# Optimization experiments

Hardware: AMD Instinct MI355X
Metric: run time of the kernel (lower is better)

## Reference

```python
import jax, jax.numpy as jnp
import numpy as np
import math

V, P, D, L, H = 50257, 1024, 768, 12, 12
HD = D // H
DFF = 4 * D
B, S = 2, 1024
EPS = 1e-5


def setup_inputs() -> dict:
    key = jax.random.key(0)
    ks = jax.random.split(key, 8)
    sc = 0.02
    return {
        "input_ids": jax.random.randint(ks[0], (B, S), 0, V),
        "wte": jax.random.normal(ks[1], (V, D), jnp.float32) * sc,
        "wpe": jax.random.normal(ks[2], (P, D), jnp.float32) * sc,
        "ln1_g": jnp.ones((L, D), jnp.float32),
        "ln1_b": jnp.zeros((L, D), jnp.float32),
        "qkv_w": jax.random.normal(ks[3], (L, 3 * D, D), jnp.float32) * sc,
        "qkv_b": jnp.zeros((L, 3 * D), jnp.float32),
        "proj_w": jax.random.normal(ks[4], (L, D, D), jnp.float32) * sc,
        "proj_b": jnp.zeros((L, D), jnp.float32),
        "ln2_g": jnp.ones((L, D), jnp.float32),
        "ln2_b": jnp.zeros((L, D), jnp.float32),
        "fc_w": jax.random.normal(ks[5], (L, DFF, D), jnp.float32) * sc,
        "fc_b": jnp.zeros((L, DFF), jnp.float32),
        "cproj_w": jax.random.normal(ks[6], (L, D, DFF), jnp.float32) * sc,
        "cproj_b": jnp.zeros((L, D), jnp.float32),
        "lnf_g": jnp.ones((D,), jnp.float32),
        "lnf_b": jnp.zeros((D,), jnp.float32),
    }


def layer_norm(x, g, b):
    mu = jnp.mean(x, axis=-1, keepdims=True)
    var = jnp.mean(jnp.square(x - mu), axis=-1, keepdims=True)
    return (x - mu) * jax.lax.rsqrt(var + EPS) * g + b


def _forward(input_ids, wte, wpe, ln1_g, ln1_b, qkv_w, qkv_b, proj_w, proj_b,
             ln2_g, ln2_b, fc_w, fc_b, cproj_w, cproj_b, lnf_g, lnf_b):
    s = input_ids.shape[1]
    h = wte[input_ids] + wpe[jnp.arange(s)][None, :, :]  # [B,S,D]
    causal = jnp.tril(jnp.ones((s, s), bool))  # [S,S]
    neg_inf = jnp.finfo(h.dtype).min

    def step(x, p):
        l1g, l1b, qw, qb, pw, pb, l2g, l2b, fw, fb, cw, cb = p
        hn = layer_norm(x, l1g, l1b)
        qkv = hn @ qw.T + qb  # [B,S,3D]
        q, k, v = jnp.split(qkv, 3, axis=-1)
        q = q.reshape(B, s, H, HD).transpose(0, 2, 1, 3)  # [B,H,S,hd]
        k = k.reshape(B, s, H, HD).transpose(0, 2, 1, 3)
        v = v.reshape(B, s, H, HD).transpose(0, 2, 1, 3)
        scores = jnp.einsum("bhqd,bhkd->bhqk", q, k) / math.sqrt(HD)
        scores = jnp.where(causal[None, None], scores, neg_inf)
        attn = jax.nn.softmax(scores, axis=-1)
        o = jnp.einsum("bhqk,bhkd->bhqd", attn, v)
        o = o.transpose(0, 2, 1, 3).reshape(B, s, D)
        x = x + (o @ pw.T + pb)
        hn2 = layer_norm(x, l2g, l2b)
        m = jax.nn.gelu(hn2 @ fw.T + fb, approximate=False)
        x = x + (m @ cw.T + cb)
        return x, None

    params = (ln1_g, ln1_b, qkv_w, qkv_b, proj_w, proj_b,
              ln2_g, ln2_b, fc_w, fc_b, cproj_w, cproj_b)
    h, _ = jax.lax.scan(step, h, params)
    h = layer_norm(h, lnf_g, lnf_b)
    logits = h @ wte.T  # tied lm_head, [B,S,V]
    return logits


def reference(input_ids, wte, wpe, ln1_g, ln1_b, qkv_w, qkv_b, proj_w, proj_b,
              ln2_g, ln2_b, fc_w, fc_b, cproj_w, cproj_b, lnf_g, lnf_b):
    return _forward(input_ids, wte, wpe, ln1_g, ln1_b, qkv_w, qkv_b, proj_w,
                    proj_b, ln2_g, ln2_b, fc_w, fc_b, cproj_w, cproj_b,
                    lnf_g, lnf_b)
```

## Files before the change

### kernel.cpp

```cpp
#include <hip/hip_runtime.h>

#define BB 2
#define SS 1024
#define DM 768
#define NH 12
#define HDIM 64
#define NL 12
#define DFFN 3072
#define VOC 50257
#define ROWS (BB * SS)
#define MT (ROWS / 128)

typedef __attribute__((ext_vector_type(4))) float f32x4;
typedef __attribute__((ext_vector_type(8))) short short8;
typedef __attribute__((ext_vector_type(4))) short short4v;
typedef unsigned short ushort;

__device__ __forceinline__ ushort f2bf(float f) {
  union { float f; unsigned int u; } x; x.f = f;
  unsigned int u = x.u;
  unsigned int r = (u + 0x7FFFu + ((u >> 16) & 1u)) >> 16;
  return (ushort)r;
}

__global__ __launch_bounds__(256) void embed_k(const int* __restrict__ ids,
    const float* __restrict__ wte, const float* __restrict__ wpe,
    float* __restrict__ h) {
  const int row = blockIdx.x;
  const int s = row & (SS - 1);
  const int tid = threadIdx.x;
  const int id = ids[row];
  const size_t wbase = (size_t)id * DM;
  const size_t pbase = (size_t)s * DM;
  const size_t obase = (size_t)row * DM;
  h[obase + tid]       = wte[wbase + tid]       + wpe[pbase + tid];
  h[obase + tid + 256] = wte[wbase + tid + 256] + wpe[pbase + tid + 256];
  h[obase + tid + 512] = wte[wbase + tid + 512] + wpe[pbase + tid + 512];
}

__global__ __launch_bounds__(256) void f2b_k(const float* __restrict__ in,
                                             ushort* __restrict__ out, int n4) {
  for (int i = blockIdx.x * 256 + threadIdx.x; i < n4; i += gridDim.x * 256) {
    f32x4 v = ((const f32x4*)in)[i];
    short4v s;
    s[0] = f2bf(v[0]); s[1] = f2bf(v[1]); s[2] = f2bf(v[2]); s[3] = f2bf(v[3]);
    ((short4v*)out)[i] = s;
  }
}

template <int OB>
__global__ __launch_bounds__(256) void layernorm_t(const float* __restrict__ x,
    const float* __restrict__ g, const float* __restrict__ b, void* __restrict__ y) {
  const int tid = threadIdx.x;
  const size_t base = (size_t)blockIdx.x * DM;
  float v0 = x[base + tid], v1 = x[base + tid + 256], v2 = x[base + tid + 512];
  __shared__ float red[256];
  red[tid] = v0 + v1 + v2;
  __syncthreads();
  for (int off = 128; off > 0; off >>= 1) {
    if (tid < off) red[tid] += red[tid + off];
    __syncthreads();
  }
  float mu = red[0] * (1.0f / DM);
  __syncthreads();
  float d0 = v0 - mu, d1 = v1 - mu, d2 = v2 - mu;
  red[tid] = d0 * d0 + d1 * d1 + d2 * d2;
  __syncthreads();
  for (int off = 128; off > 0; off >>= 1) {
    if (tid < off) red[tid] += red[tid + off];
    __syncthreads();
  }
  float rstd = rsqrtf(red[0] * (1.0f / DM) + 1e-5f);
  float o0 = d0 * rstd * g[tid]       + b[tid];
  float o1 = d1 * rstd * g[tid + 256] + b[tid + 256];
  float o2 = d2 * rstd * g[tid + 512] + b[tid + 512];
  if (OB) {
    ushort* yo = (ushort*)y;
    yo[base + tid] = f2bf(o0); yo[base + tid + 256] = f2bf(o1);
    yo[base + tid + 512] = f2bf(o2);
  } else {
    float* yo = (float*)y;
    yo[base + tid] = o0; yo[base + tid + 256] = o1; yo[base + tid + 512] = o2;
  }
}

template <int ROUNDS>
__device__ __forceinline__ void stage_sw(const ushort* __restrict__ g, int ldg,
                                         ushort* lds, int wave, int lane,
                                         int rowmax) {
#pragma unroll
  for (int r = 0; r < ROUNDS; r++) {
    const int chunk = (r * 4 + wave) * 64 + lane;
    const int nrow = chunk >> 3;
    const int cs = (chunk & 7) ^ (nrow & 7);
    const int row = nrow > rowmax ? rowmax : nrow;
    const ushort* ga = g + (size_t)row * ldg + cs * 8;
    ushort* la = lds + (r * 4 + wave) * 512;
    __builtin_amdgcn_global_load_lds(
        (const __attribute__((address_space(1))) unsigned int*)ga,
        (__attribute__((address_space(3))) unsigned int*)la, 16, 0, 0);
  }
}

__global__ __launch_bounds__(256) void gemm_lg(const ushort* __restrict__ A,
    const ushort* __restrict__ Bw, float* __restrict__ Cout, int N, int K) {
  __shared__ __align__(16) ushort smem[4 * 8192];
  ushort* AsL0 = smem;
  ushort* AsL1 = smem + 8192;
  ushort* BsL0 = smem + 16384;
  ushort* BsL1 = smem + 24576;

  const int tid = threadIdx.x;
  const int lane = tid & 63;
  const int wave = tid >> 6;
  const int la = lane & 15;
  const int hi = lane >> 4;
  const int swz = (la & 7) << 3;

  const int nwg = gridDim.x;
  int bid = blockIdx.x;
  {
    const int q = nwg >> 3, r = nwg & 7;
    const int xcd = bid & 7, idx = bid >> 3;
    bid = (xcd < r ? xcd * (q + 1) : r * (q + 1) + (xcd - r) * q) + idx;
  }
  const int m0 = (bid % MT) * 128;
  const int n0 = (bid / MT) * 128;

  const int wr = (wave >> 1) * 64;
  const int wc = (wave & 1) * 64;
  const int brmax = min(N - n0 - 1, 127);

  f32x4 acc[4][4];
#pragma unroll
  for (int i = 0; i < 4; i++)
#pragma unroll
    for (int j = 0; j < 4; j++) acc[i][j] = (f32x4){0.f, 0.f, 0.f, 0.f};

  const ushort* Ag = A + (size_t)m0 * K;
  const ushort* Bg = Bw + (size_t)n0 * K;

  const int nt = K >> 6;
  const int s0 = (bid % MT) % nt;

  stage_sw<4>(Ag + s0 * 64, K, AsL0, wave, lane, 127);
  stage_sw<4>(Bg + s0 * 64, K, BsL0, wave, lane, brmax);

  int cur = 0;
  for (int t = 0; t < nt; t++) {
    if (t + 1 < nt) {
      int sn = t + 1 + s0; if (sn >= nt) sn -= nt;
      stage_sw<4>(Ag + sn * 64, K, cur ? AsL0 : AsL1, wave, lane, 127);
      stage_sw<4>(Bg + sn * 64, K, cur ? BsL0 : BsL1, wave, lane, brmax);
      asm volatile("s_waitcnt vmcnt(8)" ::: "memory");
    } else {
      asm volatile("s_waitcnt vmcnt(0)" ::: "memory");
    }
    __builtin_amdgcn_s_barrier();
    __builtin_amdgcn_sched_barrier(0);

    const ushort* Ab = (cur ? AsL1 : AsL0) + (wr + la) * 64;
    const ushort* Bb = (cur ? BsL1 : BsL0) + (wc + la) * 64;
    __builtin_amdgcn_s_setprio(1);
#pragma unroll
    for (int ks = 0; ks < 2; ks++) {
      const int co = (ks * 32 + hi * 8) ^ swz;
      short8 a[4], b[4];
#pragma unroll
      for (int mi = 0; mi < 4; mi++)
        a[mi] = *(const short8*)(Ab + mi * 1024 + co);
#pragma unroll
      for (int ni = 0; ni < 4; ni++)
        b[ni] = *(const short8*)(Bb + ni * 1024 + co);
#pragma unroll
      for (int mi = 0; mi < 4; mi++)
#pragma unroll
        for (int ni = 0; ni < 4; ni++)
          acc[mi][ni] = __builtin_amdgcn_mfma_f32_16x16x32_bf16(
              a[mi], b[ni], acc[mi][ni], 0, 0, 0);
    }
    __builtin_amdgcn_s_setprio(0);
    __builtin_amdgcn_sched_barrier(0);
    __builtin_amdgcn_s_barrier();
    __builtin_amdgcn_sched_barrier(0);
    cur ^= 1;
  }

  float* L = (float*)smem;
  const int myhalf = wave & 1;
#pragma unroll
  for (int h = 0; h < 2; h++) {
    if (myhalf == h) {
#pragma unroll
      for (int mi = 0; mi < 4; mi++)
#pragma unroll
        for (int ni = 0; ni < 4; ni++)
#pragma unroll
          for (int j = 0; j < 4; j++) {
            const int row = wr + mi * 16 + 4 * hi + j;
            const int col = ni * 16 + la;
            L[row * 68 + col] = acc[mi][ni][j];
          }
    }
    __syncthreads();
#pragma unroll
    for (int it = 0; it < 32; it++) {
      const int flat = it * 256 + tid;
      const int row = flat >> 6, col = flat & 63;
      const int gc = n0 + h * 64 + col;
      if (gc < N)
        Cout[(size_t)(m0 + row) * N + gc] = L[row * 68 + col];
    }
    __syncthreads();
  }
}

template <int EPI, int OUTBF, int MR>
__global__ __launch_bounds__(256) void gemm_p3(const ushort* __restrict__ A,
    const ushort* __restrict__ Bw, const float* __restrict__ bias,
    const float* __restrict__ res, void* __restrict__ Cout, int N, int K) {
  constexpr int MROWS = MR * 32;
  constexpr int MTILES = ROWS / MROWS;
  constexpr int ASZ = MROWS * 64;
  constexpr int BSZ = 64 * 64;
  __shared__ __align__(16) ushort smem[3 * ASZ + 3 * BSZ];
  ushort* As = smem;
  ushort* Bs = smem + 3 * ASZ;

  const int tid = threadIdx.x;
  const int lane = tid & 63;
  const int wave = tid >> 6;
  const int la = lane & 15;
  const int hi = lane >> 4;
  const int swz = (la & 7) << 3;

  const int nwg = gridDim.x;
  int bid = blockIdx.x;
  {
    const int q = nwg >> 3, r = nwg & 7;
    const int xcd = bid & 7, idx = bid >> 3;
    bid = (xcd < r ? xcd * (q + 1) : r * (q + 1) + (xcd - r) * q) + idx;
  }
  const int m0 = (bid % MTILES) * MROWS;
  const int n0 = (bid / MTILES) * 64;

  const int wr = (wave >> 1) * (MROWS / 2);
  const int wc = (wave & 1) * 32;

  f32x4 acc[MR][2];
#pragma unroll
  for (int i = 0; i < MR; i++)
#pragma unroll
    for (int j = 0; j < 2; j++) acc[i][j] = (f32x4){0.f, 0.f, 0.f, 0.f};

  const ushort* Ag = A + (size_t)m0 * K;
  const ushort* Bg = Bw + (size_t)n0 * K;
  const int nt = K >> 6;
  const int s0 = (bid % MTILES) % nt;

  {
    int s1 = s0 + 1; if (s1 >= nt) s1 -= nt;
    stage_sw<MR>(Ag + s0 * 64, K, As, wave, lane, MROWS - 1);
    stage_sw<2>(Bg + s0 * 64, K, Bs, wave, lane, 63);
    stage_sw<MR>(Ag + s1 * 64, K, As + ASZ, wave, lane, MROWS - 1);
    stage_sw<2>(Bg + s1 * 64, K, Bs + BSZ, wave, lane, 63);
  }

  for (int t = 0; t < nt; t++) {
    if (t + 1 < nt) {
      asm volatile("s_waitcnt vmcnt(%0)" :: "i"(MR + 2) : "memory");
    } else {
      asm volatile("s_waitcnt vmcnt(0)" ::: "memory");
    }
    __builtin_amdgcn_s_barrier();
    __builtin_amdgcn_sched_barrier(0);

    const ushort* Ab = As + (t % 3) * ASZ + (wr + la) * 64;
    const ushort* Bb = Bs + (t % 3) * BSZ + (wc + la) * 64;
    __builtin_amdgcn_s_setprio(1);
#pragma unroll
    for (int ks = 0; ks < 2; ks++) {
      const int co = (ks * 32 + hi * 8) ^ swz;
      short8 a[MR], b[2];
#pragma unroll
      for (int mi = 0; mi < MR; mi++)
        a[mi] = *(const short8*)(Ab + mi * 1024 + co);
#pragma unroll
      for (int ni = 0; ni < 2; ni++)
        b[ni] = *(const short8*)(Bb + ni * 1024 + co);
#pragma unroll
      for (int mi = 0; mi < MR; mi++)
#pragma unroll
        for (int ni = 0; ni < 2; ni++)
          acc[mi][ni] = __builtin_amdgcn_mfma_f32_16x16x32_bf16(
              a[mi], b[ni], acc[mi][ni], 0, 0, 0);
    }
    __builtin_amdgcn_s_setprio(0);
    __builtin_amdgcn_sched_barrier(0);
    __builtin_amdgcn_s_barrier();
    __builtin_amdgcn_sched_barrier(0);
    if (t + 2 < nt) {
      int sn = t + 2 + s0; if (sn >= nt) sn -= nt;
      stage_sw<MR>(Ag + sn * 64, K, As + ((t + 2) % 3) * ASZ, wave, lane, MROWS - 1);
      stage_sw<2>(Bg + sn * 64, K, Bs + ((t + 2) % 3) * BSZ, wave, lane, 63);
    }
  }

  if (OUTBF) {
    ushort* L = smem;
#pragma unroll
    for (int mi = 0; mi < MR; mi++)
#pragma unroll
      for (int ni = 0; ni < 2; ni++)
#pragma unroll
        for (int j = 0; j < 4; j++) {
          const int row = wr + mi * 16 + 4 * hi + j;
          const int col = wc + ni * 16 + la;
          float x = acc[mi][ni][j];
          if (EPI >= 1) x += bias[n0 + col];
          if (EPI == 3) x = 0.5f * x * (1.0f + erff(x * 0.70710678118f));
          L[row * 72 + col] = f2bf(x);
        }
    __syncthreads();
    ushort* Co = (ushort*)Cout;
    constexpr int ITERS = MROWS * 64 / 8 / 256;
#pragma unroll
    for (int it = 0; it < ITERS; it++) {
      const int idx8 = it * 256 + tid;
      const int row = idx8 >> 3, c8 = idx8 & 7;
      short8 v = *(const short8*)&L[row * 72 + c8 * 8];
      *(short8*)&Co[(size_t)(m0 + row) * N + n0 + c8 * 8] = v;
    }
  } else {
    float* L = (float*)smem;
#pragma unroll
    for (int mi = 0; mi < MR; mi++)
#pragma unroll
      for (int ni = 0; ni < 2; ni++)
#pragma unroll
        for (int j = 0; j < 4; j++) {
          const int row = wr + mi * 16 + 4 * hi + j;
          const int col = wc + ni * 16 + la;
          float x = acc[mi][ni][j];
          if (EPI >= 1) x += bias[n0 + col];
          if (EPI == 3) x = 0.5f * x * (1.0f + erff(x * 0.70710678118f));
          L[row * 68 + col] = x;
        }
    __syncthreads();
    f32x4* Co = (f32x4*)Cout;
    const f32x4* R4 = (const f32x4*)res;
    constexpr int ITERS = MROWS * 64 / 4 / 256;
#pragma unroll
    for (int it = 0; it < ITERS; it++) {
      const int idx4 = it * 256 + tid;
      const int row = idx4 >> 4, c4 = idx4 & 15;
      f32x4 v = *(const f32x4*)&L[row * 68 + c4 * 4];
      const size_t o4 = ((size_t)(m0 + row) * N + n0) / 4 + c4;
      if (EPI == 2) v += R4[o4];
      Co[o4] = v;
    }
  }
}

__global__ __launch_bounds__(256) void attn_bf(const ushort* __restrict__ qkv,
                                               ushort* __restrict__ o) {
  const int tid = threadIdx.x;
  const int lane = tid & 63;
  const int wave = tid >> 6;
  const int hi = lane >> 4;
  const int la = lane & 15;
  const int q0 = blockIdx.x * 64;
  const int bh = blockIdx.y;
  const int bb = bh / NH;
  const int hh = bh % NH;
  const size_t rstride = 3 * DM;
  const ushort* base = qkv + (size_t)bb * SS * rstride;
  const ushort* kbase = base + DM + hh * HDIM;
  const ushort* vbase = base + 2 * DM + hh * HDIM;

  __shared__ ushort Ks[64][72];
  __shared__ ushort Vt[64][72];
  __shared__ ushort Pb[4][16][72];

  const int kr = tid >> 2;
  const int kc = (tid & 3) * 16;
  const int vp0 = (tid >> 3) * 2;
  const int vc = (tid & 7) * 8;

  short8 qf[2];
  {
    const int qrow = q0 + wave * 16 + la;
    const ushort* qp = base + (size_t)qrow * rstride + hh * HDIM + 8 * hi;
    qf[0] = *(const short8*)qp;
    qf[1] = *(const short8*)(qp + 32);
  }

  short8 kA, kB, vA, vB;
  {
    const ushort* kp = kbase + (size_t)kr * rstride + kc;
    kA = *(const short8*)kp;
    kB = *(const short8*)(kp + 8);
    const ushort* vp = vbase + (size_t)vp0 * rstride + vc;
    vA = *(const short8*)vp;
    vB = *(const short8*)(vp + rstride);
  }

  f32x4 accO[4] = {};
  float m_[4], l_[4];
#pragma unroll
  for (int j = 0; j < 4; j++) { m_[j] = -1e30f; l_[j] = 0.f; }

  const int nt = q0 / 64 + 1;
  for (int kt = 0; kt < nt; kt++) {
    __syncthreads();
    *(short8*)&Ks[kr][kc]     = kA;
    *(short8*)&Ks[kr][kc + 8] = kB;
#pragma unroll
    for (int i = 0; i < 8; i++) {
      unsigned int pk = (unsigned int)(unsigned short)vA[i] |
                        ((unsigned int)(unsigned short)vB[i] << 16);
      *(unsigned int*)&Vt[vc + i][vp0] = pk;
    }
    __syncthreads();
    if (kt + 1 < nt) {
      const ushort* kp = kbase + (size_t)((kt + 1) * 64 + kr) * rstride + kc;
      kA = *(const short8*)kp;
      kB = *(const short8*)(kp + 8);
      const ushort* vp = vbase + (size_t)((kt + 1) * 64 + vp0) * rstride + vc;
      vA = *(const short8*)vp;
      vB = *(const short8*)(vp + rstride);
    }

    f32x4 s[4] = {};
#pragma unroll
    for (int f = 0; f < 4; f++) {
#pragma unroll
      for (int kk = 0; kk < 2; kk++) {
        short8 kf = *(const short8*)&Ks[f * 16 + la][kk * 32 + 8 * hi];
        s[f] = __builtin_amdgcn_mfma_f32_16x16x32_bf16(qf[kk], kf, s[f], 0, 0, 0);
      }
#pragma unroll
      for (int j = 0; j < 4; j++) s[f][j] *= 0.125f;
    }

    if (kt == nt - 1) {
      const int qr = wave * 16 + 4 * hi;
#pragma unroll
      for (int f = 0; f < 4; f++) {
        const int kcol = f * 16 + la;
#pragma unroll
        for (int j = 0; j < 4; j++)
          if (kcol > qr + j) s[f][j] = -1e30f;
      }
    }

#pragma unroll
    for (int j = 0; j < 4; j++) {
      float rm = fmaxf(fmaxf(s[0][j], s[1][j]), fmaxf(s[2][j], s[3][j]));
      rm = fmaxf(rm, __shfl_xor(rm, 1));
      rm = fmaxf(rm, __shfl_xor(rm, 2));
      rm = fmaxf(rm, __shfl_xor(rm, 4));
      rm = fmaxf(rm, __shfl_xor(rm, 8));
      const float mnew = fmaxf(m_[j], rm);
      const float alpha = expf(m_[j] - mnew);
      float rs = 0.f;
#pragma unroll
      for (int f = 0; f < 4; f++) {
        const float p = expf(s[f][j] - mnew);
        s[f][j] = p;
        rs += p;
      }
      rs += __shfl_xor(rs, 1);
      rs += __shfl_xor(rs, 2);
      rs += __shfl_xor(rs, 4);
      rs += __shfl_xor(rs, 8);
      l_[j] = l_[j] * alpha + rs;
      m_[j] = mnew;
#pragma unroll
      for (int f = 0; f < 4; f++) accO[f][j] *= alpha;
    }

#pragma unroll
    for (int f = 0; f < 4; f++)
#pragma unroll
      for (int j = 0; j < 4; j++)
        Pb[wave][4 * hi + j][f * 16 + la] = f2bf(s[f][j]);

    short8 pf0 = *(const short8*)&Pb[wave][la][8 * hi];
    short8 pf1 = *(const short8*)&Pb[wave][la][32 + 8 * hi];
#pragma unroll
    for (int f = 0; f < 4; f++) {
      short8 vf0 = *(const short8*)&Vt[f * 16 + la][8 * hi];
      short8 vf1 = *(const short8*)&Vt[f * 16 + la][32 + 8 * hi];
      accO[f] = __builtin_amdgcn_mfma_f32_16x16x32_bf16(pf0, vf0, accO[f], 0, 0, 0);
      accO[f] = __builtin_amdgcn_mfma_f32_16x16x32_bf16(pf1, vf1, accO[f], 0, 0, 0);
    }
  }

  ushort* op = o + (size_t)(bb * SS + q0 + wave * 16) * DM + hh * HDIM;
#pragma unroll
  for (int j = 0; j < 4; j++) {
    const float inv = 1.0f / l_[j];
    const int qr = 4 * hi + j;
#pragma unroll
    for (int f = 0; f < 4; f++)
      op[(size_t)qr * DM + f * 16 + la] = f2bf(accO[f][j] * inv);
  }
}

template <int EPI>
__global__ __launch_bounds__(256) void gemm_nt(const float* __restrict__ A,
    const float* __restrict__ Bw, const float* __restrict__ bias,
    const float* __restrict__ res, float* __restrict__ C, int N, int K) {
  __shared__ ushort As[64][40];
  __shared__ ushort Bs[64][40];
  const int tid = threadIdx.x;
  const int m0 = blockIdx.y * 64;
  const int n0 = blockIdx.x * 64;
  const int lane = tid & 63;
  const int wave = tid >> 6;
  const int wr = (wave >> 1) * 32;
  const int wc = (wave & 1) * 32;
  const int lr = lane & 15;
  const int lk = (lane >> 4) * 8;
  const int sr = tid >> 2;
  const int sc = (tid & 3) * 8;
  f32x4 acc[2][2] = {};
  for (int kk = 0; kk < K; kk += 32) {
    {
      const float* p = A + (size_t)(m0 + sr) * K + kk + sc;
      f32x4 v0 = *(const f32x4*)p;
      f32x4 v1 = *(const f32x4*)(p + 4);
      short8 sv;
      for (int i = 0; i < 4; i++) { sv[i] = f2bf(v0[i]); sv[4 + i] = f2bf(v1[i]); }
      *(short8*)&As[sr][sc] = sv;
    }
    {
      const int gr = n0 + sr;
      short8 sv = {};
      if (gr < N) {
        const float* p = Bw + (size_t)gr * K + kk + sc;
        f32x4 v0 = *(const f32x4*)p;
        f32x4 v1 = *(const f32x4*)(p + 4);
        for (int i = 0; i < 4; i++) { sv[i] = f2bf(v0[i]); sv[4 + i] = f2bf(v1[i]); }
      }
      *(short8*)&Bs[sr][sc] = sv;
    }
    __syncthreads();
    short8 a0 = *(const short8*)&As[wr + lr][lk];
    short8 a1 = *(const short8*)&As[wr + 16 + lr][lk];
    short8 b0 = *(const short8*)&Bs[wc + lr][lk];
    short8 b1 = *(const short8*)&Bs[wc + 16 + lr][lk];
    acc[0][0] = __builtin_amdgcn_mfma_f32_16x16x32_bf16(a0, b0, acc[0][0], 0, 0, 0);
    acc[0][1] = __builtin_amdgcn_mfma_f32_16x16x32_bf16(a0, b1, acc[0][1], 0, 0, 0);
    acc[1][0] = __builtin_amdgcn_mfma_f32_16x16x32_bf16(a1, b0, acc[1][0], 0, 0, 0);
    acc[1][1] = __builtin_amdgcn_mfma_f32_16x16x32_bf16(a1, b1, acc[1][1], 0, 0, 0);
    __syncthreads();
  }
  const int orow = (lane >> 4) * 4;
  for (int mi = 0; mi < 2; mi++)
    for (int ni = 0; ni < 2; ni++) {
      const int col = n0 + wc + ni * 16 + lr;
      if (col >= N) continue;
      for (int j = 0; j < 4; j++) {
        const int row = m0 + wr + mi * 16 + orow + j;
        float x = acc[mi][ni][j];
        if (EPI >= 1) x += bias[col];
        const size_t idx = (size_t)row * N + col;
        if (EPI == 2) x += res[idx];
        if (EPI == 3) x = 0.5f * x * (1.0f + erff(x * 0.70710678118f));
        C[idx] = x;
      }
    }
}

__global__ __launch_bounds__(256) void attn_f32(const float* __restrict__ qkv,
                                                float* __restrict__ o) {
  const int tid = threadIdx.x;
  const int lane = tid & 63;
  const int wave = tid >> 6;
  const int hi = lane >> 4;
  const int la = lane & 15;
  const int q0 = blockIdx.x * 64;
  const int bh = blockIdx.y;
  const int bb = bh / NH;
  const int hh = bh % NH;
  const size_t rstride = 3 * DM;
  const float* base = qkv + (size_t)bb * SS * rstride;
  __shared__ ushort Ks[64][72];
  __shared__ ushort Vt[64][72];
  __shared__ ushort Pb[4][16][72];
  short8 qf[2];
  {
    const int qrow = q0 + wave * 16 + la;
    const float* qp = base + (size_t)qrow * rstride + hh * HDIM + 8 * hi;
    for (int kk = 0; kk < 2; kk++) {
      f32x4 v0 = *(const f32x4*)(qp + 32 * kk);
      f32x4 v1 = *(const f32x4*)(qp + 32 * kk + 4);
      short8 sv;
      for (int i = 0; i < 4; i++) {
        sv[i] = f2bf(v0[i] * 0.125f); sv[4 + i] = f2bf(v1[i] * 0.125f);
      }
      qf[kk] = sv;
    }
  }
  f32x4 accO[4] = {};
  float m_[4], l_[4];
  for (int j = 0; j < 4; j++) { m_[j] = -1e30f; l_[j] = 0.f; }
  const int nt = q0 / 64 + 1;
  for (int kt = 0; kt < nt; kt++) {
    __syncthreads();
    {
      const int r = tid >> 2;
      const int c = (tid & 3) * 16;
      const float* kp = base + (size_t)(kt * 64 + r) * rstride + DM + hh * HDIM + c;
      const float* vp = kp + DM;
      f32x4 k0 = *(const f32x4*)kp, k1 = *(const f32x4*)(kp + 4);
      f32x4 k2 = *(const f32x4*)(kp + 8), k3 = *(const f32x4*)(kp + 12);
      short8 s0, s1;
      for (int i = 0; i < 4; i++) {
        s0[i] = f2bf(k0[i]); s0[4 + i] = f2bf(k1[i]);
        s1[i] = f2bf(k2[i]); s1[4 + i] = f2bf(k3[i]);
      }
      *(short8*)&Ks[r][c] = s0;
      *(short8*)&Ks[r][c + 8] = s1;
      f32x4 v0 = *(const f32x4*)vp, v1 = *(const f32x4*)(vp + 4);
      f32x4 v2 = *(const f32x4*)(vp + 8), v3 = *(const f32x4*)(vp + 12);
      for (int i = 0; i < 4; i++) {
        Vt[c + i][r] = f2bf(v0[i]); Vt[c + 4 + i][r] = f2bf(v1[i]);
        Vt[c + 8 + i][r] = f2bf(v2[i]); Vt[c + 12 + i][r] = f2bf(v3[i]);
      }
    }
    __syncthreads();
    f32x4 s[4] = {};
    for (int f = 0; f < 4; f++)
      for (int kk = 0; kk < 2; kk++) {
        short8 kf = *(const short8*)&Ks[f * 16 + la][kk * 32 + 8 * hi];
        s[f] = __builtin_amdgcn_mfma_f32_16x16x32_bf16(qf[kk], kf, s[f], 0, 0, 0);
      }
    if (kt == nt - 1) {
      const int qr = wave * 16 + 4 * hi;
      for (int f = 0; f < 4; f++) {
        const int kcol = f * 16 + la;
        for (int j = 0; j < 4; j++)
          if (kcol > qr + j) s[f][j] = -1e30f;
      }
    }
    for (int j = 0; j < 4; j++) {
      float rm = fmaxf(fmaxf(s[0][j], s[1][j]), fmaxf(s[2][j], s[3][j]));
      rm = fmaxf(rm, __shfl_xor(rm, 1));
      rm = fmaxf(rm, __shfl_xor(rm, 2));
      rm = fmaxf(rm, __shfl_xor(rm, 4));
      rm = fmaxf(rm, __shfl_xor(rm, 8));
      const float mnew = fmaxf(m_[j], rm);
      const float alpha = expf(m_[j] - mnew);
      float rs = 0.f;
      for (int f = 0; f < 4; f++) {
        const float p = expf(s[f][j] - mnew);
        s[f][j] = p; rs += p;
      }
      rs += __shfl_xor(rs, 1);
      rs += __shfl_xor(rs, 2);
      rs += __shfl_xor(rs, 4);
      rs += __shfl_xor(rs, 8);
      l_[j] = l_[j] * alpha + rs;
      m_[j] = mnew;
      for (int f = 0; f < 4; f++) accO[f][j] *= alpha;
    }
    for (int f = 0; f < 4; f++)
      for (int j = 0; j < 4; j++)
        Pb[wave][4 * hi + j][f * 16 + la] = f2bf(s[f][j]);
    short8 pf0 = *(const short8*)&Pb[wave][la][8 * hi];
    short8 pf1 = *(const short8*)&Pb[wave][la][32 + 8 * hi];
    for (int f = 0; f < 4; f++) {
      short8 vf0 = *(const short8*)&Vt[f * 16 + la][8 * hi];
      short8 vf1 = *(const short8*)&Vt[f * 16 + la][32 + 8 * hi];
      accO[f] = __builtin_amdgcn_mfma_f32_16x16x32_bf16(pf0, vf0, accO[f], 0, 0, 0);
      accO[f] = __builtin_amdgcn_mfma_f32_16x16x32_bf16(pf1, vf1, accO[f], 0, 0, 0);
    }
  }
  float* op = o + (size_t)(bb * SS + q0 + wave * 16) * DM + hh * HDIM;
  for (int j = 0; j < 4; j++) {
    const float inv = 1.0f / l_[j];
    const int qr = 4 * hi + j;
    for (int f = 0; f < 4; f++)
      op[(size_t)qr * DM + f * 16 + la] = accO[f][j] * inv;
  }
}

extern "C" void kernel_launch(void* const* d_in, const int* in_sizes, int n_in,
                              void* d_out, int out_size, void* d_ws,
                              size_t ws_size, hipStream_t stream) {
  const int*   ids     = (const int*)d_in[0];
  const float* wte     = (const float*)d_in[1];
  const float* wpe     = (const float*)d_in[2];
  const float* ln1_g   = (const float*)d_in[3];
  const float* ln1_b   = (const float*)d_in[4];
  const float* qkv_w   = (const float*)d_in[5];
  const float* qkv_b   = (const float*)d_in[6];
  const float* proj_w  = (const float*)d_in[7];
  const float* proj_b  = (const float*)d_in[8];
  const float* ln2_g   = (const float*)d_in[9];
  const float* ln2_b   = (const float*)d_in[10];
  const float* fc_w    = (const float*)d_in[11];
  const float* fc_b    = (const float*)d_in[12];
  const float* cproj_w = (const float*)d_in[13];
  const float* cproj_b = (const float*)d_in[14];
  const float* lnf_g   = (const float*)d_in[15];
  const float* lnf_b   = (const float*)d_in[16];
  float* out = (float*)d_out;

  const size_t sz_h    = (size_t)ROWS * DM * 4;
  const size_t sz_hn   = (size_t)ROWS * DM * 2;
  const size_t sz_qkv  = (size_t)ROWS * 3 * DM * 2;
  const size_t sz_ob   = (size_t)ROWS * DM * 2;
  const size_t sz_mb   = (size_t)ROWS * DFFN * 2;
  const size_t sz_wq   = (size_t)NL * 3 * DM * DM * 2;
  const size_t sz_wp   = (size_t)NL * DM * DM * 2;
  const size_t sz_wf   = (size_t)NL * DFFN * DM * 2;
  const size_t sz_wc   = (size_t)NL * DM * DFFN * 2;
  const size_t sz_wt   = (size_t)VOC * DM * 2;
  const size_t NEED = sz_h + sz_hn + sz_qkv + sz_ob + sz_mb +
                      sz_wq + sz_wp + sz_wf + sz_wc + sz_wt;

  if (ws_size >= NEED) {
    char* p = (char*)d_ws;
    float*  h    = (float*)p;  p += sz_h;
    ushort* hn   = (ushort*)p; p += sz_hn;
    ushort* qkvb = (ushort*)p; p += sz_qkv;
    ushort* ob   = (ushort*)p; p += sz_ob;
    ushort* mb   = (ushort*)p; p += sz_mb;
    ushort* wq   = (ushort*)p; p += sz_wq;
    ushort* wp   = (ushort*)p; p += sz_wp;
    ushort* wf   = (ushort*)p; p += sz_wf;
    ushort* wc   = (ushort*)p; p += sz_wc;
    ushort* wt   = (ushort*)p; p += sz_wt;

    f2b_k<<<2048, 256, 0, stream>>>(qkv_w,   wq, NL * 3 * DM * DM / 4);
    f2b_k<<<1024, 256, 0, stream>>>(proj_w,  wp, NL * DM * DM / 4);
    f2b_k<<<2048, 256, 0, stream>>>(fc_w,    wf, NL * DFFN * DM / 4);
    f2b_k<<<2048, 256, 0, stream>>>(cproj_w, wc, NL * DM * DFFN / 4);
    f2b_k<<<2048, 256, 0, stream>>>(wte,     wt, VOC * DM / 4);

    embed_k<<<ROWS, 256, 0, stream>>>(ids, wte, wpe, h);

    for (int l = 0; l < NL; l++) {
      layernorm_t<1><<<ROWS, 256, 0, stream>>>(h, ln1_g + l * DM, ln1_b + l * DM, hn);
      gemm_p3<1, 1, 4><<<MT * (3 * DM / 64), 256, 0, stream>>>(
          hn, wq + (size_t)l * 3 * DM * DM, qkv_b + (size_t)l * 3 * DM,
          nullptr, qkvb, 3 * DM, DM);
      attn_bf<<<dim3(SS / 64, BB * NH), 256, 0, stream>>>(qkvb, ob);
      gemm_p3<2, 0, 2><<<(ROWS / 64) * (DM / 64), 256, 0, stream>>>(
          ob, wp + (size_t)l * DM * DM, proj_b + (size_t)l * DM, h, h, DM, DM);
      layernorm_t<1><<<ROWS, 256, 0, stream>>>(h, ln2_g + l * DM, ln2_b + l * DM, hn);
      gemm_p3<3, 1, 4><<<MT * (DFFN / 64), 256, 0, stream>>>(
          hn, wf + (size_t)l * DFFN * DM, fc_b + (size_t)l * DFFN,
          nullptr, mb, DFFN, DM);
      gemm_p3<2, 0, 2><<<(ROWS / 64) * (DM / 64), 256, 0, stream>>>(
          mb, wc + (size_t)l * DM * DFFN, cproj_b + (size_t)l * DM, h, h,
          DM, DFFN);
    }

    layernorm_t<1><<<ROWS, 256, 0, stream>>>(h, lnf_g, lnf_b, hn);
    gemm_lg<<<MT * ((VOC + 127) / 128), 256, 0, stream>>>(
        hn, wt, out, VOC, DM);
  } else {
    float* ws = (float*)d_ws;
    float* h   = ws;
    float* hn  = h + (size_t)ROWS * DM;
    float* qkv = hn + (size_t)ROWS * DM;
    float* ob  = qkv + (size_t)ROWS * 3 * DM;
    float* mb  = ob + (size_t)ROWS * DM;

    embed_k<<<ROWS, 256, 0, stream>>>(ids, wte, wpe, h);
    for (int l = 0; l < NL; l++) {
      layernorm_t<0><<<ROWS, 256, 0, stream>>>(h, ln1_g + l * DM, ln1_b + l * DM, hn);
      gemm_nt<1><<<dim3(3 * DM / 64, ROWS / 64), 256, 0, stream>>>(
          hn, qkv_w + (size_t)l * 3 * DM * DM, qkv_b + (size_t)l * 3 * DM,
          nullptr, qkv, 3 * DM, DM);
      attn_f32<<<dim3(SS / 64, BB * NH), 256, 0, stream>>>(qkv, ob);
      gemm_nt<2><<<dim3(DM / 64, ROWS / 64), 256, 0, stream>>>(
          ob, proj_w + (size_t)l * DM * DM, proj_b + (size_t)l * DM, h, h, DM, DM);
      layernorm_t<0><<<ROWS, 256, 0, stream>>>(h, ln2_g + l * DM, ln2_b + l * DM, hn);
      gemm_nt<3><<<dim3(DFFN / 64, ROWS / 64), 256, 0, stream>>>(
          hn, fc_w + (size_t)l * DFFN * DM, fc_b + (size_t)l * DFFN,
          nullptr, mb, DFFN, DM);
      gemm_nt<2><<<dim3(DM / 64, ROWS / 64), 256, 0, stream>>>(
          mb, cproj_w + (size_t)l * DM * DFFN, cproj_b + (size_t)l * DM, h, h,
          DM, DFFN);
    }
    layernorm_t<0><<<ROWS, 256, 0, stream>>>(h, lnf_g, lnf_b, hn);
    gemm_nt<0><<<dim3((VOC + 63) / 64, ROWS / 64), 256, 0, stream>>>(
        hn, wte, nullptr, nullptr, out, VOC, DM);
  }
}
```

Before: 2.036 ms.

## Use 256x256 tiles with 512-thread blocks for the LM-head GEMM

```diff
diff --git a/kernel.cpp b/kernel.cpp
--- a/kernel.cpp
+++ b/kernel.cpp
@@ -102,13 +102,30 @@
   }
 }
 
-__global__ __launch_bounds__(256) void gemm_lg(const ushort* __restrict__ A,
+template <int ROUNDS>
+__device__ __forceinline__ void stage8(const ushort* __restrict__ g, int ldg,
+                                       ushort* lds, int wave, int lane,
+                                       int rowmax) {
+#pragma unroll
+  for (int r = 0; r < ROUNDS; r++) {
+    const int chunk = (r * 8 + wave) * 64 + lane;
+    const int nrow = chunk >> 3;
+    const int cs = (chunk & 7) ^ (nrow & 7);
+    const int row = nrow > rowmax ? rowmax : nrow;
+    const ushort* ga = g + (size_t)row * ldg + cs * 8;
+    ushort* la = lds + (r * 8 + wave) * 512;
+    __builtin_amdgcn_global_load_lds(
+        (const __attribute__((address_space(1))) unsigned int*)ga,
+        (__attribute__((address_space(3))) unsigned int*)la, 16, 0, 0);
+  }
+}
+
+__global__ __launch_bounds__(512, 2) void gemm_256(const ushort* __restrict__ A,
     const ushort* __restrict__ Bw, float* __restrict__ Cout, int N, int K) {
-  __shared__ __align__(16) ushort smem[4 * 8192];
-  ushort* AsL0 = smem;
-  ushort* AsL1 = smem + 8192;
-  ushort* BsL0 = smem + 16384;
-  ushort* BsL1 = smem + 24576;
+  constexpr int TSZ = 256 * 64;
+  __shared__ __align__(16) ushort smem[4 * TSZ];
+  ushort* As = smem;
+  ushort* Bs = smem + 2 * TSZ;
 
   const int tid = threadIdx.x;
   const int lane = tid & 63;
@@ -116,6 +133,8 @@
   const int la = lane & 15;
   const int hi = lane >> 4;
   const int swz = (la & 7) << 3;
+  const int wr2 = wave >> 2;
+  const int wc2 = wave & 3;
 
   const int nwg = gridDim.x;
   int bid = blockIdx.x;
@@ -124,34 +143,30 @@
     const int xcd = bid & 7, idx = bid >> 3;
     bid = (xcd < r ? xcd * (q + 1) : r * (q + 1) + (xcd - r) * q) + idx;
   }
-  const int m0 = (bid % MT) * 128;
-  const int n0 = (bid / MT) * 128;
-
-  const int wr = (wave >> 1) * 64;
-  const int wc = (wave & 1) * 64;
-  const int brmax = min(N - n0 - 1, 127);
-
-  f32x4 acc[4][4];
-#pragma unroll
-  for (int i = 0; i < 4; i++)
+  const int m0 = (bid & 7) * 256;
+  const int n0 = (bid >> 3) * 256;
+  const int brmax = min(N - n0 - 1, 255);
+
+  f32x4 acc[8][4];
+#pragma unroll
+  for (int i = 0; i < 8; i++)
 #pragma unroll
     for (int j = 0; j < 4; j++) acc[i][j] = (f32x4){0.f, 0.f, 0.f, 0.f};
 
   const ushort* Ag = A + (size_t)m0 * K;
   const ushort* Bg = Bw + (size_t)n0 * K;
-
   const int nt = K >> 6;
-  const int s0 = (bid % MT) % nt;
-
-  stage_sw<4>(Ag + s0 * 64, K, AsL0, wave, lane, 127);
-  stage_sw<4>(Bg + s0 * 64, K, BsL0, wave, lane, brmax);
+  const int s0 = bid % nt;
+
+  stage8<4>(Ag + s0 * 64, K, As, wave, lane, 255);
+  stage8<4>(Bg + s0 * 64, K, Bs, wave, lane, brmax);
 
   int cur = 0;
   for (int t = 0; t < nt; t++) {
     if (t + 1 < nt) {
       int sn = t + 1 + s0; if (sn >= nt) sn -= nt;
-      stage_sw<4>(Ag + sn * 64, K, cur ? AsL0 : AsL1, wave, lane, 127);
-      stage_sw<4>(Bg + sn * 64, K, cur ? BsL0 : BsL1, wave, lane, brmax);
+      stage8<4>(Ag + sn * 64, K, As + (cur ^ 1) * TSZ, wave, lane, 255);
+      stage8<4>(Bg + sn * 64, K, Bs + (cur ^ 1) * TSZ, wave, lane, brmax);
       asm volatile("s_waitcnt vmcnt(8)" ::: "memory");
     } else {
       asm volatile("s_waitcnt vmcnt(0)" ::: "memory");
@@ -159,21 +174,21 @@
     __builtin_amdgcn_s_barrier();
     __builtin_amdgcn_sched_barrier(0);
 
-    const ushort* Ab = (cur ? AsL1 : AsL0) + (wr + la) * 64;
-    const ushort* Bb = (cur ? BsL1 : BsL0) + (wc + la) * 64;
+    const ushort* Ab = As + cur * TSZ + (wr2 * 128 + la) * 64;
+    const ushort* Bb = Bs + cur * TSZ + (wc2 * 64 + la) * 64;
     __builtin_amdgcn_s_setprio(1);
 #pragma unroll
     for (int ks = 0; ks < 2; ks++) {
       const int co = (ks * 32 + hi * 8) ^ swz;
-      short8 a[4], b[4];
-#pragma unroll
-      for (int mi = 0; mi < 4; mi++)
+      short8 a[8], b[4];
+#pragma unroll
+      for (int mi = 0; mi < 8; mi++)
         a[mi] = *(const short8*)(Ab + mi * 1024 + co);
 #pragma unroll
       for (int ni = 0; ni < 4; ni++)
         b[ni] = *(const short8*)(Bb + ni * 1024 + co);
 #pragma unroll
-      for (int mi = 0; mi < 4; mi++)
+      for (int mi = 0; mi < 8; mi++)
 #pragma unroll
         for (int ni = 0; ni < 4; ni++)
           acc[mi][ni] = __builtin_amdgcn_mfma_f32_16x16x32_bf16(
@@ -187,17 +202,16 @@
   }
 
   float* L = (float*)smem;
-  const int myhalf = wave & 1;
-#pragma unroll
-  for (int h = 0; h < 2; h++) {
-    if (myhalf == h) {
-#pragma unroll
-      for (int mi = 0; mi < 4; mi++)
+#pragma unroll
+  for (int p = 0; p < 4; p++) {
+    if (wc2 == p) {
+#pragma unroll
+      for (int mi = 0; mi < 8; mi++)
 #pragma unroll
         for (int ni = 0; ni < 4; ni++)
 #pragma unroll
           for (int j = 0; j < 4; j++) {
-            const int row = wr + mi * 16 + 4 * hi + j;
+            const int row = wr2 * 128 + mi * 16 + 4 * hi + j;
             const int col = ni * 16 + la;
             L[row * 68 + col] = acc[mi][ni][j];
           }
@@ -205,9 +219,9 @@
     __syncthreads();
 #pragma unroll
     for (int it = 0; it < 32; it++) {
-      const int flat = it * 256 + tid;
+      const int flat = it * 512 + tid;
       const int row = flat >> 6, col = flat & 63;
-      const int gc = n0 + h * 64 + col;
+      const int gc = n0 + p * 64 + col;
       if (gc < N)
         Cout[(size_t)(m0 + row) * N + gc] = L[row * 68 + col];
     }
@@ -762,7 +776,7 @@
     }
 
     layernorm_t<1><<<ROWS, 256, 0, stream>>>(h, lnf_g, lnf_b, hn);
-    gemm_lg<<<MT * ((VOC + 127) / 128), 256, 0, stream>>>(
+    gemm_256<<<8 * ((VOC + 255) / 256), 512, 0, stream>>>(
         hn, wt, out, VOC, DM);
   } else {
     float* ws = (float*)d_ws;
```

New measurement: 2.066 ms. No clear change (+1.5%).
